# Optimization experiments

Measured on AMD Instinct MI355X. Metric: run time of the kernel, lower is better.

Reference implementation:

```python
import jax, jax.numpy as jnp
import numpy as np

N, L, H, K, T = 768, 8, 64, 4, 3

def _mlp2(x, w1, b1, w2, b2):
    # Linear -> ReLU -> Linear -> ReLU (matches nn.Sequential in q/k/v MLPs)
    return jax.nn.relu(jax.nn.relu(x @ w1 + b1) @ w2 + b2)

def setup_inputs() -> dict:
    key = jax.random.key(0)
    ks = jax.random.split(key, 20)
    s = 1.0 / np.sqrt(H)
    def lin(k, din, dout):
        return jax.random.uniform(k, (din, dout), jnp.float32, -s, s)
    def bias(k, dout):
        return jax.random.uniform(k, (dout,), jnp.float32, -s, s)
    inp = {
        "h": jax.random.normal(ks[0], (N, L, H), jnp.float32),
        "coord": jax.random.normal(ks[1], (N, L, K, T), jnp.float32),
        "wq1": lin(ks[2], H, H), "bq1": bias(ks[3], H),
        "wq2": lin(ks[4], H, H), "bq2": bias(ks[5], H),
        "wk1": lin(ks[6], H, H), "bk1": bias(ks[7], H),
        "wk2": lin(ks[8], H, H), "bk2": bias(ks[9], H),
        "wv1": lin(ks[10], H, H), "bv1": bias(ks[11], H),
        "wv2": lin(ks[12], H, H), "bv2": bias(ks[13], H),
        "wc1": lin(ks[14], H, H), "bc1": bias(ks[15], H),
        # final coord layer: Linear(H, 4, bias=False), xavier gain=0.001
        "wc2": jax.random.normal(ks[16], (H, K), jnp.float32) * 0.001,
    }
    return inp

def reference(h, coord, wq1, bq1, wq2, bq2, wk1, bk1, wk2, bk2,
              wv1, bv1, wv2, bv2, wc1, bc1, wc2):
    q = _mlp2(h, wq1, bq1, wq2, bq2)          # [N, L, H]
    k = _mlp2(h, wk1, bk1, wk2, bk2)          # [N, L, H]
    v = _mlp2(h, wv1, bv1, wv2, bv2)          # [N, L, H]
    # scores[i, j, l] = <q_i, k_j> per frame l; softmax over neighbor axis j (dim=1)
    scores = jnp.einsum('ilh,jlh->ijl', q, k)
    alpha = jax.nn.softmax(scores, axis=1)     # [N, N, L]
    h_agg = jnp.einsum('ijl,jlh->ilh', alpha, v)
    cmv = jax.nn.relu(v @ wc1 + bc1) @ wc2     # coord_mlp(v): [N, L, 4]
    coord_diff = coord[:, None] - coord[None]  # [N, N, L, 4, 3]
    x_agg = jnp.einsum('ijlkt,ijl,jlk->ilkt', coord_diff, alpha, cmv)
    return (h + h_agg, coord + x_agg)
```

## Files before the change

### kernel.cpp

```cpp
#include <hip/hip_runtime.h>
#include <hip/hip_bf16.h>

#define NN 768
#define LL 8
#define HH 64
#define QR 16
#define IT 16
#define SCP 772
#define ABP 776

typedef __attribute__((ext_vector_type(8))) short bf16x8;
typedef __attribute__((ext_vector_type(4))) float f32x4;

__device__ __forceinline__ short f2bf(float x) {
    union { __hip_bfloat16 h; short s; } u;
    u.h = __float2bfloat16(x);
    return u.s;
}

__device__ __forceinline__ bf16x8 pack8(float4 lo, float4 hi) {
    bf16x8 r;
    r[0] = f2bf(lo.x); r[1] = f2bf(lo.y); r[2] = f2bf(lo.z); r[3] = f2bf(lo.w);
    r[4] = f2bf(hi.x); r[5] = f2bf(hi.y); r[6] = f2bf(hi.z); r[7] = f2bf(hi.w);
    return r;
}

__device__ __forceinline__ void layer16(const float (*IN)[68], int rbase, int k0,
                                        int c4, const float* __restrict__ W,
                                        const float* __restrict__ b,
                                        float4 res[4]) {
    float4 acc[4] = {{0,0,0,0},{0,0,0,0},{0,0,0,0},{0,0,0,0}};
    #pragma unroll
    for (int kk = 0; kk < 16; ++kk) {
        const int k = k0 + kk;
        const float4 wv = *(const float4*)&W[k * 64 + c4];
        #pragma unroll
        for (int rr = 0; rr < 4; ++rr) {
            const float xv = IN[rbase + rr][k];
            acc[rr].x = fmaf(xv, wv.x, acc[rr].x);
            acc[rr].y = fmaf(xv, wv.y, acc[rr].y);
            acc[rr].z = fmaf(xv, wv.z, acc[rr].z);
            acc[rr].w = fmaf(xv, wv.w, acc[rr].w);
        }
    }
    const float4 bb = *(const float4*)&b[c4];
    #pragma unroll
    for (int rr = 0; rr < 4; ++rr) {
        acc[rr].x += __shfl_xor(acc[rr].x, 16, 64);
        acc[rr].x += __shfl_xor(acc[rr].x, 32, 64);
        acc[rr].y += __shfl_xor(acc[rr].y, 16, 64);
        acc[rr].y += __shfl_xor(acc[rr].y, 32, 64);
        acc[rr].z += __shfl_xor(acc[rr].z, 16, 64);
        acc[rr].z += __shfl_xor(acc[rr].z, 32, 64);
        acc[rr].w += __shfl_xor(acc[rr].w, 16, 64);
        acc[rr].w += __shfl_xor(acc[rr].w, 32, 64);
        res[rr].x = fmaxf(acc[rr].x + bb.x, 0.f);
        res[rr].y = fmaxf(acc[rr].y + bb.y, 0.f);
        res[rr].z = fmaxf(acc[rr].z + bb.z, 0.f);
        res[rr].w = fmaxf(acc[rr].w + bb.w, 0.f);
    }
}

__global__ __launch_bounds__(256) void qkv_kernel(
    const float* __restrict__ h, const float* __restrict__ coord,
    const float* __restrict__ wq1, const float* __restrict__ bq1,
    const float* __restrict__ wq2, const float* __restrict__ bq2,
    const float* __restrict__ wk1, const float* __restrict__ bk1,
    const float* __restrict__ wk2, const float* __restrict__ bk2,
    const float* __restrict__ wv1, const float* __restrict__ bv1,
    const float* __restrict__ wv2, const float* __restrict__ bv2,
    const float* __restrict__ wc1, const float* __restrict__ bc1,
    const float* __restrict__ wc2,
    float* __restrict__ q_ws, float* __restrict__ k_ws,
    float* __restrict__ vT_ws, float* __restrict__ UT_ws)
{
    const int t     = threadIdx.x;
    const int c4    = (t & 15) * 4;
    const int ks    = (t >> 4) & 3;
    const int k0    = ks * 16;
    const int rbase = (t >> 6) * 4;
    const bool lead = (ks == 0);
    const int r0    = blockIdx.x * QR;

    __shared__ float A[QR][68];
    __shared__ float B[QR][68];

    *(float4*)&A[t >> 4][(t & 15) * 4] =
        *(const float4*)&h[(r0 + (t >> 4)) * 64 + (t & 15) * 4];
    __syncthreads();

    float4 res[4];

    layer16(A, rbase, k0, c4, wq1, bq1, res);
    if (lead) {
        #pragma unroll
        for (int rr = 0; rr < 4; ++rr) *(float4*)&B[rbase + rr][c4] = res[rr];
    }
    __syncthreads();
    layer16(B, rbase, k0, c4, wq2, bq2, res);
    if (lead) {
        #pragma unroll
        for (int rr = 0; rr < 4; ++rr) {
            const int g = r0 + rbase + rr, i = g >> 3, l = g & 7;
            *(float4*)&q_ws[(l * NN + i) * 64 + c4] = res[rr];
        }
    }
    __syncthreads();

    layer16(A, rbase, k0, c4, wk1, bk1, res);
    if (lead) {
        #pragma unroll
        for (int rr = 0; rr < 4; ++rr) *(float4*)&B[rbase + rr][c4] = res[rr];
    }
    __syncthreads();
    layer16(B, rbase, k0, c4, wk2, bk2, res);
    if (lead) {
        #pragma unroll
        for (int rr = 0; rr < 4; ++rr) {
            const int g = r0 + rbase + rr, i = g >> 3, l = g & 7;
            *(float4*)&k_ws[(l * NN + i) * 64 + c4] = res[rr];
        }
    }
    __syncthreads();

    layer16(A, rbase, k0, c4, wv1, bv1, res);
    if (lead) {
        #pragma unroll
        for (int rr = 0; rr < 4; ++rr) *(float4*)&B[rbase + rr][c4] = res[rr];
    }
    __syncthreads();
    layer16(B, rbase, k0, c4, wv2, bv2, res);
    if (lead) {
        #pragma unroll
        for (int rr = 0; rr < 4; ++rr) {
            const int g = r0 + rbase + rr, i = g >> 3, l = g & 7;
            vT_ws[((size_t)l * 64 + c4 + 0) * NN + i] = res[rr].x;
            vT_ws[((size_t)l * 64 + c4 + 1) * NN + i] = res[rr].y;
            vT_ws[((size_t)l * 64 + c4 + 2) * NN + i] = res[rr].z;
            vT_ws[((size_t)l * 64 + c4 + 3) * NN + i] = res[rr].w;
            *(float4*)&A[rbase + rr][c4] = res[rr];
        }
    }
    __syncthreads();

    layer16(A, rbase, k0, c4, wc1, bc1, res);
    if (lead) {
        #pragma unroll
        for (int rr = 0; rr < 4; ++rr) *(float4*)&B[rbase + rr][c4] = res[rr];
    }
    __syncthreads();
    {
        const int row = t >> 4;
        const int kk  = (t >> 2) & 3;
        const int seg = t & 3;
        float p = 0.f;
        #pragma unroll
        for (int k2 = 0; k2 < 16; ++k2) {
            const int k = seg * 16 + k2;
            p = fmaf(B[row][k], wc2[k * 4 + kk], p);
        }
        p += __shfl_xor(p, 1, 64);
        p += __shfl_xor(p, 2, 64);
        const int g = r0 + row, i = g >> 3, l = g & 7;
        const float uval =
            (seg == 0) ? p : p * coord[g * 12 + kk * 3 + (seg - 1)];
        UT_ws[((size_t)l * 16 + kk * 4 + seg) * NN + i] = uval;
    }
}

__global__ __launch_bounds__(256) void attn_kernel(
    const float* __restrict__ q_ws, const float* __restrict__ k_ws,
    const float* __restrict__ vT_ws, const float* __restrict__ UT_ws,
    const float* __restrict__ h, const float* __restrict__ coord,
    float* __restrict__ h_out, float* __restrict__ x_out)
{
    const int l    = blockIdx.x & 7;
    const int i0   = (blockIdx.x >> 3) * IT;
    const int t    = threadIdx.x;
    const int lane = t & 63;
    const int w    = t >> 6;
    const int m    = lane & 15;
    const int quad = lane >> 4;

    __shared__ float sc[IT][SCP];
    __shared__ alignas(16) short al[IT][ABP];
    __shared__ float rinv_s[IT];
    __shared__ float part3[4][IT][16];
    __shared__ float smS[IT][16];

    bf16x8 aq0, aq1;
    {
        const float* qrow = q_ws + ((size_t)l * NN + i0 + m) * 64 + quad * 8;
        aq0 = pack8(*(const float4*)qrow,        *(const float4*)(qrow + 4));
        aq1 = pack8(*(const float4*)(qrow + 32), *(const float4*)(qrow + 36));
    }

    {
        const float* kl = k_ws + (size_t)l * NN * 64;
        for (int nt = 0; nt < 12; ++nt) {
            const int jb = 192 * w + nt * 16;
            const float* krow = kl + (size_t)(jb + m) * 64 + quad * 8;
            bf16x8 b0 = pack8(*(const float4*)krow,        *(const float4*)(krow + 4));
            bf16x8 b1 = pack8(*(const float4*)(krow + 32), *(const float4*)(krow + 36));
            f32x4 d = {0.f, 0.f, 0.f, 0.f};
            d = __builtin_amdgcn_mfma_f32_16x16x32_bf16(aq0, b0, d, 0, 0, 0);
            d = __builtin_amdgcn_mfma_f32_16x16x32_bf16(aq1, b1, d, 0, 0, 0);
            #pragma unroll
            for (int rg = 0; rg < 4; ++rg)
                sc[quad * 4 + rg][jb + m] = d[rg];
        }
    }
    __syncthreads();

    {
        const int row = t >> 4, sub = t & 15;
        float mx = -1e30f;
        for (int n = 0; n < 48; ++n) mx = fmaxf(mx, sc[row][sub + 16 * n]);
        mx = fmaxf(mx, __shfl_xor(mx, 1, 64));
        mx = fmaxf(mx, __shfl_xor(mx, 2, 64));
        mx = fmaxf(mx, __shfl_xor(mx, 4, 64));
        mx = fmaxf(mx, __shfl_xor(mx, 8, 64));
        float s = 0.f;
        for (int n = 0; n < 48; ++n) {
            const int j = sub + 16 * n;
            const float e = __expf(sc[row][j] - mx);
            s += e;
            al[row][j] = f2bf(e);
        }
        s += __shfl_xor(s, 1, 64);
        s += __shfl_xor(s, 2, 64);
        s += __shfl_xor(s, 4, 64);
        s += __shfl_xor(s, 8, 64);
        if (sub == 0) rinv_s[row] = 1.f / s;
    }
    __syncthreads();

    {
        f32x4 acc = {0.f, 0.f, 0.f, 0.f};
        const float* vrow = vT_ws + ((size_t)l * 64 + 16 * w + m) * NN;
        #pragma unroll 4
        for (int kt = 0; kt < 24; ++kt) {
            const int k0 = kt * 32;
            bf16x8 a = *(const bf16x8*)&al[m][k0 + quad * 8];
            bf16x8 b = pack8(*(const float4*)(vrow + k0 + quad * 8),
                             *(const float4*)(vrow + k0 + quad * 8 + 4));
            acc = __builtin_amdgcn_mfma_f32_16x16x32_bf16(a, b, acc, 0, 0, 0);
        }
        const int c = 16 * w + m;
        #pragma unroll
        for (int rg = 0; rg < 4; ++rg) {
            const int i = quad * 4 + rg;
            const int row = ((i0 + i) * 8 + l) * 64 + c;
            h_out[row] = h[row] + rinv_s[i] * acc[rg];
        }
    }

    {
        f32x4 acc = {0.f, 0.f, 0.f, 0.f};
        const float* urow = UT_ws + ((size_t)l * 16 + m) * NN + 192 * w;
        #pragma unroll
        for (int kt = 0; kt < 6; ++kt) {
            const int k0 = kt * 32;
            bf16x8 a = *(const bf16x8*)&al[m][192 * w + k0 + quad * 8];
            bf16x8 b = pack8(*(const float4*)(urow + k0 + quad * 8),
                             *(const float4*)(urow + k0 + quad * 8 + 4));
            acc = __builtin_amdgcn_mfma_f32_16x16x32_bf16(a, b, acc, 0, 0, 0);
        }
        #pragma unroll
        for (int rg = 0; rg < 4; ++rg)
            part3[w][quad * 4 + rg][m] = acc[rg];
    }
    __syncthreads();
    {
        const int i = t >> 4, u = t & 15;
        smS[i][u] = (part3[0][i][u] + part3[1][i][u] +
                     part3[2][i][u] + part3[3][i][u]) * rinv_s[i];
    }
    __syncthreads();
    if (t < 192) {
        const int i4 = t / 12, kt = t % 12, k4 = kt / 3, s4 = kt % 3;
        const int idx = ((i0 + i4) * 8 + l) * 12 + kt;
        const float cd = coord[idx];
        x_out[idx] = cd + cd * smS[i4][k4 * 4] - smS[i4][k4 * 4 + 1 + s4];
    }
}

extern "C" void kernel_launch(void* const* d_in, const int* in_sizes, int n_in,
                              void* d_out, int out_size, void* d_ws, size_t ws_size,
                              hipStream_t stream) {
    const float* h     = (const float*)d_in[0];
    const float* coord = (const float*)d_in[1];

    float* h_out = (float*)d_out;
    float* x_out = h_out + NN * LL * HH;

    float* q_ws  = (float*)d_ws;
    float* k_ws  = q_ws + NN * LL * HH;
    float* vT_ws = k_ws + NN * LL * HH;
    float* UT_ws = vT_ws + NN * LL * HH;

    qkv_kernel<<<(NN * LL) / QR, 256, 0, stream>>>(
        h, coord,
        (const float*)d_in[2],  (const float*)d_in[3],
        (const float*)d_in[4],  (const float*)d_in[5],
        (const float*)d_in[6],  (const float*)d_in[7],
        (const float*)d_in[8],  (const float*)d_in[9],
        (const float*)d_in[10], (const float*)d_in[11],
        (const float*)d_in[12], (const float*)d_in[13],
        (const float*)d_in[14], (const float*)d_in[15],
        (const float*)d_in[16],
        q_ws, k_ws, vT_ws, UT_ws);

    attn_kernel<<<(NN / IT) * LL, 256, 0, stream>>>(
        q_ws, k_ws, vT_ws, UT_ws, h, coord, h_out, x_out);
}
```

Before: 135.5 us.

## Split q/k/v MLP chains across waves and store intermediates as bf16

The projection kernel now assigns each wave one of three independent chains (q, k, or v plus coord MLP) over 4 rows, using wave barriers instead of block-wide syncthreads, and launches 1152 blocks. The workspace tensors q, k, vT and U are written as bf16, so the attention kernel loads bf16x8 directly instead of loading fp32 and packing. This cuts workspace traffic roughly in half and removes conversion work and block syncs. In exchange the v-chain waves do more work than the q and k waves, which causes load imbalance, and U is now rounded to bf16 at the store rather than when loaded.

```diff
diff --git a/kernel.cpp b/kernel.cpp
--- a/kernel.cpp
+++ b/kernel.cpp
@@ -4,7 +4,6 @@
 #define NN 768
 #define LL 8
 #define HH 64
-#define QR 16
 #define IT 16
 #define SCP 772
 #define ABP 776
@@ -18,17 +17,10 @@
     return u.s;
 }
 
-__device__ __forceinline__ bf16x8 pack8(float4 lo, float4 hi) {
-    bf16x8 r;
-    r[0] = f2bf(lo.x); r[1] = f2bf(lo.y); r[2] = f2bf(lo.z); r[3] = f2bf(lo.w);
-    r[4] = f2bf(hi.x); r[5] = f2bf(hi.y); r[6] = f2bf(hi.z); r[7] = f2bf(hi.w);
-    return r;
-}
-
-__device__ __forceinline__ void layer16(const float (*IN)[68], int rbase, int k0,
-                                        int c4, const float* __restrict__ W,
-                                        const float* __restrict__ b,
-                                        float4 res[4]) {
+__device__ __forceinline__ void layer4(const float (*IN)[68], int k0, int c4,
+                                       const float* __restrict__ W,
+                                       const float* __restrict__ b,
+                                       float4 res[4]) {
     float4 acc[4] = {{0,0,0,0},{0,0,0,0},{0,0,0,0},{0,0,0,0}};
     #pragma unroll
     for (int kk = 0; kk < 16; ++kk) {
@@ -36,7 +28,7 @@
         const float4 wv = *(const float4*)&W[k * 64 + c4];
         #pragma unroll
         for (int rr = 0; rr < 4; ++rr) {
-            const float xv = IN[rbase + rr][k];
+            const float xv = IN[rr][k];
             acc[rr].x = fmaf(xv, wv.x, acc[rr].x);
             acc[rr].y = fmaf(xv, wv.y, acc[rr].y);
             acc[rr].z = fmaf(xv, wv.z, acc[rr].z);
@@ -71,106 +63,119 @@
     const float* __restrict__ wv2, const float* __restrict__ bv2,
     const float* __restrict__ wc1, const float* __restrict__ bc1,
     const float* __restrict__ wc2,
-    float* __restrict__ q_ws, float* __restrict__ k_ws,
-    float* __restrict__ vT_ws, float* __restrict__ UT_ws)
+    short* __restrict__ q_ws, short* __restrict__ k_ws,
+    short* __restrict__ vT_ws, short* __restrict__ UT_ws)
 {
-    const int t     = threadIdx.x;
-    const int c4    = (t & 15) * 4;
-    const int ks    = (t >> 4) & 3;
-    const int k0    = ks * 16;
-    const int rbase = (t >> 6) * 4;
+    const int lane  = threadIdx.x & 63;
+    const int w     = threadIdx.x >> 6;
+    const int wid   = blockIdx.x * 4 + w;
+    const int chain = wid / 1536;
+    const int rg    = wid - chain * 1536;
+    const int r0    = rg * 4;
+
+    const int c4   = (lane & 15) * 4;
+    const int ks   = (lane >> 4) & 3;
+    const int k0   = ks * 16;
     const bool lead = (ks == 0);
-    const int r0    = blockIdx.x * QR;
-
-    __shared__ float A[QR][68];
-    __shared__ float B[QR][68];
-
-    *(float4*)&A[t >> 4][(t & 15) * 4] =
-        *(const float4*)&h[(r0 + (t >> 4)) * 64 + (t & 15) * 4];
-    __syncthreads();
+
+    __shared__ float As[4][4][68];
+    __shared__ float Bs[4][4][68];
+    float (*A)[68] = As[w];
+    float (*B)[68] = Bs[w];
+
+    {
+        const int row = lane >> 4;
+        *(float4*)&A[row][c4] = *(const float4*)&h[(r0 + row) * 64 + c4];
+    }
+    __builtin_amdgcn_wave_barrier();
 
     float4 res[4];
 
-    layer16(A, rbase, k0, c4, wq1, bq1, res);
-    if (lead) {
-        #pragma unroll
-        for (int rr = 0; rr < 4; ++rr) *(float4*)&B[rbase + rr][c4] = res[rr];
-    }
-    __syncthreads();
-    layer16(B, rbase, k0, c4, wq2, bq2, res);
-    if (lead) {
-        #pragma unroll
-        for (int rr = 0; rr < 4; ++rr) {
-            const int g = r0 + rbase + rr, i = g >> 3, l = g & 7;
-            *(float4*)&q_ws[(l * NN + i) * 64 + c4] = res[rr];
-        }
-    }
-    __syncthreads();
-
-    layer16(A, rbase, k0, c4, wk1, bk1, res);
-    if (lead) {
-        #pragma unroll
-        for (int rr = 0; rr < 4; ++rr) *(float4*)&B[rbase + rr][c4] = res[rr];
-    }
-    __syncthreads();
-    layer16(B, rbase, k0, c4, wk2, bk2, res);
-    if (lead) {
-        #pragma unroll
-        for (int rr = 0; rr < 4; ++rr) {
-            const int g = r0 + rbase + rr, i = g >> 3, l = g & 7;
-            *(float4*)&k_ws[(l * NN + i) * 64 + c4] = res[rr];
-        }
-    }
-    __syncthreads();
-
-    layer16(A, rbase, k0, c4, wv1, bv1, res);
-    if (lead) {
-        #pragma unroll
-        for (int rr = 0; rr < 4; ++rr) *(float4*)&B[rbase + rr][c4] = res[rr];
-    }
-    __syncthreads();
-    layer16(B, rbase, k0, c4, wv2, bv2, res);
-    if (lead) {
-        #pragma unroll
-        for (int rr = 0; rr < 4; ++rr) {
-            const int g = r0 + rbase + rr, i = g >> 3, l = g & 7;
-            vT_ws[((size_t)l * 64 + c4 + 0) * NN + i] = res[rr].x;
-            vT_ws[((size_t)l * 64 + c4 + 1) * NN + i] = res[rr].y;
-            vT_ws[((size_t)l * 64 + c4 + 2) * NN + i] = res[rr].z;
-            vT_ws[((size_t)l * 64 + c4 + 3) * NN + i] = res[rr].w;
-            *(float4*)&A[rbase + rr][c4] = res[rr];
-        }
-    }
-    __syncthreads();
-
-    layer16(A, rbase, k0, c4, wc1, bc1, res);
-    if (lead) {
-        #pragma unroll
-        for (int rr = 0; rr < 4; ++rr) *(float4*)&B[rbase + rr][c4] = res[rr];
-    }
-    __syncthreads();
-    {
-        const int row = t >> 4;
-        const int kk  = (t >> 2) & 3;
-        const int seg = t & 3;
-        float p = 0.f;
-        #pragma unroll
-        for (int k2 = 0; k2 < 16; ++k2) {
-            const int k = seg * 16 + k2;
-            p = fmaf(B[row][k], wc2[k * 4 + kk], p);
-        }
-        p += __shfl_xor(p, 1, 64);
-        p += __shfl_xor(p, 2, 64);
-        const int g = r0 + row, i = g >> 3, l = g & 7;
-        const float uval =
-            (seg == 0) ? p : p * coord[g * 12 + kk * 3 + (seg - 1)];
-        UT_ws[((size_t)l * 16 + kk * 4 + seg) * NN + i] = uval;
+    if (chain == 0) {
+        layer4(A, k0, c4, wq1, bq1, res);
+        if (lead) {
+            #pragma unroll
+            for (int rr = 0; rr < 4; ++rr) *(float4*)&B[rr][c4] = res[rr];
+        }
+        __builtin_amdgcn_wave_barrier();
+        layer4(B, k0, c4, wq2, bq2, res);
+        if (lead) {
+            #pragma unroll
+            for (int rr = 0; rr < 4; ++rr) {
+                const int g = r0 + rr, i = g >> 3, l = g & 7;
+                short4 s;
+                s.x = f2bf(res[rr].x); s.y = f2bf(res[rr].y);
+                s.z = f2bf(res[rr].z); s.w = f2bf(res[rr].w);
+                *(short4*)&q_ws[(l * NN + i) * 64 + c4] = s;
+            }
+        }
+    } else if (chain == 1) {
+        layer4(A, k0, c4, wk1, bk1, res);
+        if (lead) {
+            #pragma unroll
+            for (int rr = 0; rr < 4; ++rr) *(float4*)&B[rr][c4] = res[rr];
+        }
+        __builtin_amdgcn_wave_barrier();
+        layer4(B, k0, c4, wk2, bk2, res);
+        if (lead) {
+            #pragma unroll
+            for (int rr = 0; rr < 4; ++rr) {
+                const int g = r0 + rr, i = g >> 3, l = g & 7;
+                short4 s;
+                s.x = f2bf(res[rr].x); s.y = f2bf(res[rr].y);
+                s.z = f2bf(res[rr].z); s.w = f2bf(res[rr].w);
+                *(short4*)&k_ws[(l * NN + i) * 64 + c4] = s;
+            }
+        }
+    } else {
+        layer4(A, k0, c4, wv1, bv1, res);
+        if (lead) {
+            #pragma unroll
+            for (int rr = 0; rr < 4; ++rr) *(float4*)&B[rr][c4] = res[rr];
+        }
+        __builtin_amdgcn_wave_barrier();
+        layer4(B, k0, c4, wv2, bv2, res);
+        if (lead) {
+            #pragma unroll
+            for (int rr = 0; rr < 4; ++rr) {
+                const int g = r0 + rr, i = g >> 3, l = g & 7;
+                vT_ws[((size_t)l * 64 + c4 + 0) * NN + i] = f2bf(res[rr].x);
+                vT_ws[((size_t)l * 64 + c4 + 1) * NN + i] = f2bf(res[rr].y);
+                vT_ws[((size_t)l * 64 + c4 + 2) * NN + i] = f2bf(res[rr].z);
+                vT_ws[((size_t)l * 64 + c4 + 3) * NN + i] = f2bf(res[rr].w);
+                *(float4*)&A[rr][c4] = res[rr];
+            }
+        }
+        __builtin_amdgcn_wave_barrier();
+        layer4(A, k0, c4, wc1, bc1, res);
+        if (lead) {
+            #pragma unroll
+            for (int rr = 0; rr < 4; ++rr) *(float4*)&B[rr][c4] = res[rr];
+        }
+        __builtin_amdgcn_wave_barrier();
+        {
+            const int row = lane >> 4;
+            const int kk  = (lane >> 2) & 3;
+            const int seg = lane & 3;
+            float p = 0.f;
+            #pragma unroll
+            for (int k2 = 0; k2 < 16; ++k2) {
+                const int k = seg * 16 + k2;
+                p = fmaf(B[row][k], wc2[k * 4 + kk], p);
+            }
+            p += __shfl_xor(p, 1, 64);
+            p += __shfl_xor(p, 2, 64);
+            const int g = r0 + row, i = g >> 3, l = g & 7;
+            const float uval =
+                (seg == 0) ? p : p * coord[g * 12 + kk * 3 + (seg - 1)];
+            UT_ws[((size_t)l * 16 + kk * 4 + seg) * NN + i] = f2bf(uval);
+        }
     }
 }
 
 __global__ __launch_bounds__(256) void attn_kernel(
-    const float* __restrict__ q_ws, const float* __restrict__ k_ws,
-    const float* __restrict__ vT_ws, const float* __restrict__ UT_ws,
+    const short* __restrict__ q_ws, const short* __restrict__ k_ws,
+    const short* __restrict__ vT_ws, const short* __restrict__ UT_ws,
     const float* __restrict__ h, const float* __restrict__ coord,
     float* __restrict__ h_out, float* __restrict__ x_out)
 {
@@ -188,20 +193,16 @@
     __shared__ float part3[4][IT][16];
     __shared__ float smS[IT][16];
 
-    bf16x8 aq0, aq1;
-    {
-        const float* qrow = q_ws + ((size_t)l * NN + i0 + m) * 64 + quad * 8;
-        aq0 = pack8(*(const float4*)qrow,        *(const float4*)(qrow + 4));
-        aq1 = pack8(*(const float4*)(qrow + 32), *(const float4*)(qrow + 36));
-    }
-
-    {
-        const float* kl = k_ws + (size_t)l * NN * 64;
+    const bf16x8 aq0 = *(const bf16x8*)&q_ws[((size_t)l * NN + i0 + m) * 64 + quad * 8];
+    const bf16x8 aq1 = *(const bf16x8*)&q_ws[((size_t)l * NN + i0 + m) * 64 + 32 + quad * 8];
+
+    {
+        const short* kl = k_ws + (size_t)l * NN * 64;
         for (int nt = 0; nt < 12; ++nt) {
             const int jb = 192 * w + nt * 16;
-            const float* krow = kl + (size_t)(jb + m) * 64 + quad * 8;
-            bf16x8 b0 = pack8(*(const float4*)krow,        *(const float4*)(krow + 4));
-            bf16x8 b1 = pack8(*(const float4*)(krow + 32), *(const float4*)(krow + 36));
+            const short* krow = kl + (size_t)(jb + m) * 64;
+            bf16x8 b0 = *(const bf16x8*)(krow + quad * 8);
+            bf16x8 b1 = *(const bf16x8*)(krow + 32 + quad * 8);
             f32x4 d = {0.f, 0.f, 0.f, 0.f};
             d = __builtin_amdgcn_mfma_f32_16x16x32_bf16(aq0, b0, d, 0, 0, 0);
             d = __builtin_amdgcn_mfma_f32_16x16x32_bf16(aq1, b1, d, 0, 0, 0);
@@ -237,13 +238,12 @@
 
     {
         f32x4 acc = {0.f, 0.f, 0.f, 0.f};
-        const float* vrow = vT_ws + ((size_t)l * 64 + 16 * w + m) * NN;
+        const short* vrow = vT_ws + ((size_t)l * 64 + 16 * w + m) * NN;
         #pragma unroll 4
         for (int kt = 0; kt < 24; ++kt) {
             const int k0 = kt * 32;
             bf16x8 a = *(const bf16x8*)&al[m][k0 + quad * 8];
-            bf16x8 b = pack8(*(const float4*)(vrow + k0 + quad * 8),
-                             *(const float4*)(vrow + k0 + quad * 8 + 4));
+            bf16x8 b = *(const bf16x8*)(vrow + k0 + quad * 8);
             acc = __builtin_amdgcn_mfma_f32_16x16x32_bf16(a, b, acc, 0, 0, 0);
         }
         const int c = 16 * w + m;
@@ -257,13 +257,12 @@
 
     {
         f32x4 acc = {0.f, 0.f, 0.f, 0.f};
-        const float* urow = UT_ws + ((size_t)l * 16 + m) * NN + 192 * w;
+        const short* urow = UT_ws + ((size_t)l * 16 + m) * NN + 192 * w;
         #pragma unroll
         for (int kt = 0; kt < 6; ++kt) {
             const int k0 = kt * 32;
             bf16x8 a = *(const bf16x8*)&al[m][192 * w + k0 + quad * 8];
-            bf16x8 b = pack8(*(const float4*)(urow + k0 + quad * 8),
-                             *(const float4*)(urow + k0 + quad * 8 + 4));
+            bf16x8 b = *(const bf16x8*)(urow + k0 + quad * 8);
             acc = __builtin_amdgcn_mfma_f32_16x16x32_bf16(a, b, acc, 0, 0, 0);
         }
         #pragma unroll
@@ -294,12 +293,12 @@
     float* h_out = (float*)d_out;
     float* x_out = h_out + NN * LL * HH;
 
-    float* q_ws  = (float*)d_ws;
-    float* k_ws  = q_ws + NN * LL * HH;
-    float* vT_ws = k_ws + NN * LL * HH;
-    float* UT_ws = vT_ws + NN * LL * HH;
-
-    qkv_kernel<<<(NN * LL) / QR, 256, 0, stream>>>(
+    short* q_ws  = (short*)d_ws;
+    short* k_ws  = q_ws + NN * LL * HH;
+    short* vT_ws = k_ws + NN * LL * HH;
+    short* UT_ws = vT_ws + NN * LL * HH;
+
+    qkv_kernel<<<1152, 256, 0, stream>>>(
         h, coord,
         (const float*)d_in[2],  (const float*)d_in[3],
         (const float*)d_in[4],  (const float*)d_in[5],
```

Result: faster. 116.8 us (-13.8%).
